# Optimization experiments

Hardware: AMD Instinct MI355X
Metric: run time of the kernel (lower is better)

The kernel has to match this reference:

```python
import jax, jax.numpy as jnp
import numpy as np

NUM_K_HEADS = 16
NUM_V_HEADS = 32
DK = 128
DV = 128
KCONV = 4
EPS = 1e-6
KEY_DIM = NUM_K_HEADS * DK      # 2048
VALUE_DIM = NUM_V_HEADS * DV    # 4096
HIDDEN = 2048
T_TOKENS = 4096


def setup_inputs() -> dict:
    key = jax.random.key(0)
    ks = jax.random.split(key, 10)
    s = 0.02
    return {
        "hidden_states": jax.random.normal(ks[0], (T_TOKENS, HIDDEN), jnp.float32),
        "W_qkv": jax.random.normal(ks[1], (2 * KEY_DIM + VALUE_DIM, HIDDEN), jnp.float32) * s,
        "W_z": jax.random.normal(ks[2], (VALUE_DIM, HIDDEN), jnp.float32) * s,
        "W_b": jax.random.normal(ks[3], (NUM_V_HEADS, HIDDEN), jnp.float32) * s,
        "W_a": jax.random.normal(ks[4], (NUM_V_HEADS, HIDDEN), jnp.float32) * s,
        "conv_weight": jax.random.normal(ks[5], (2 * KEY_DIM + VALUE_DIM, KCONV), jnp.float32) * 0.2,
        "dt_bias": jnp.ones((NUM_V_HEADS,), jnp.float32),
        "A_log": jax.random.normal(ks[6], (NUM_V_HEADS,), jnp.float32) * 0.5,
        "norm_weight": jnp.ones((DV,), jnp.float32),
        "W_out": jax.random.normal(ks[7], (HIDDEN, VALUE_DIM), jnp.float32) * s,
    }


def _l2norm(x):
    return x * jax.lax.rsqrt(jnp.sum(x * x, axis=-1, keepdims=True) + 1e-6)


def _gdn_forward(hidden_states, W_qkv, W_z, W_b, W_a, conv_weight,
                 dt_bias, A_log, norm_weight, W_out):
    T = hidden_states.shape[0]
    # input projections
    mixed_qkv = hidden_states @ W_qkv.T                         # [T, 2K+V]
    z = (hidden_states @ W_z.T).reshape(T, NUM_V_HEADS, DV)     # gate
    b = hidden_states @ W_b.T                                   # [T, Hv]
    a = hidden_states @ W_a.T                                   # [T, Hv]

    # depthwise causal conv1d (kernel 4) + silu, no bias
    xp = jnp.pad(mixed_qkv, ((KCONV - 1, 0), (0, 0)))
    conv = sum(xp[i:i + T] * conv_weight[:, i] for i in range(KCONV))
    x = jax.nn.silu(conv)

    q = x[:, :KEY_DIM].reshape(T, NUM_K_HEADS, DK)
    k = x[:, KEY_DIM:2 * KEY_DIM].reshape(T, NUM_K_HEADS, DK)
    v = x[:, 2 * KEY_DIM:].reshape(T, NUM_V_HEADS, DV)

    rep = NUM_V_HEADS // NUM_K_HEADS  # grouped value attention: repeat q/k heads
    q = jnp.repeat(_l2norm(q), rep, axis=1)  # [T, Hv, DK]
    k = jnp.repeat(_l2norm(k), rep, axis=1)

    beta = jax.nn.sigmoid(b)                                   # [T, Hv]
    g = -jnp.exp(A_log) * jax.nn.softplus(a + dt_bias)         # [T, Hv] log-decay
    scale = DK ** -0.5

    def step(S, inp):
        qt, kt, vt, bt, gt = inp
        S = S * jnp.exp(gt)[:, None, None]                     # gated decay
        kv = jnp.einsum('hk,hkv->hv', kt, S)                   # memory readout
        delta = (vt - kv) * bt[:, None]                        # delta rule update
        S = S + jnp.einsum('hk,hv->hkv', kt, delta)
        ot = jnp.einsum('hk,hkv->hv', qt, S) * scale
        return S, ot

    S0 = jnp.zeros((NUM_V_HEADS, DK, DV), mixed_qkv.dtype)
    _, o = jax.lax.scan(step, S0, (q, k, v, beta, g))          # o: [T, Hv, DV]

    # gated RMSNorm (norm before gate)
    var = jnp.mean(o * o, axis=-1, keepdims=True)
    on = o * jax.lax.rsqrt(var + EPS) * norm_weight
    y = on * jax.nn.silu(z)

    return y.reshape(T, VALUE_DIM) @ W_out.T                   # [T, HIDDEN]


def reference(hidden_states, W_qkv, W_z, W_b, W_a, conv_weight,
              dt_bias, A_log, norm_weight, W_out):
    return _gdn_forward(hidden_states, W_qkv, W_z, W_b, W_a, conv_weight,
                        dt_bias, A_log, norm_weight, W_out)
```

## Files before the change

### kernel.cpp

```cpp
#include <hip/hip_runtime.h>
#include <cstdint>
#include <cstddef>

typedef __bf16 bf16_t;
typedef __bf16 bf16x8 __attribute__((ext_vector_type(8)));
typedef __bf16 bf16x4 __attribute__((ext_vector_type(4)));
typedef float floatx4 __attribute__((ext_vector_type(4)));

__device__ __forceinline__ void async16(const bf16_t* g, bf16_t* l) {
  __builtin_amdgcn_global_load_lds(
      (const __attribute__((address_space(1))) unsigned int*)g,
      (__attribute__((address_space(3))) unsigned int*)l, 16, 0, 0);
}

__device__ __forceinline__ void barrier_lds() {
  asm volatile("s_waitcnt lgkmcnt(0)\n\ts_barrier" ::: "memory");
}

__device__ __forceinline__ float siluf(float x) { return x / (1.f + __expf(-x)); }

#define MFMA16(a, b, c) __builtin_amdgcn_mfma_f32_16x16x32_bf16(a, b, c, 0, 0, 0)

__global__ __launch_bounds__(256) void k_cvt(const float* __restrict__ in,
                                             bf16_t* __restrict__ out, int n4) {
  int i = blockIdx.x * 256 + threadIdx.x;
  if (i >= n4) return;
  const float4 f = ((const float4*)in)[i];
  bf16x4 r;
  r[0] = (bf16_t)f.x; r[1] = (bf16_t)f.y; r[2] = (bf16_t)f.z; r[3] = (bf16_t)f.w;
  ((bf16x4*)out)[i] = r;
}

__global__ __launch_bounds__(256) void k_build_wba(const float* __restrict__ wb,
                                                   const float* __restrict__ wa,
                                                   bf16_t* __restrict__ out) {
  int i = blockIdx.x * 256 + threadIdx.x;
  int e = i * 4;
  int row = e >> 11;
  int col = e & 2047;
  float4 f = make_float4(0.f, 0.f, 0.f, 0.f);
  if (row < 32)      f = *(const float4*)&wb[row * 2048 + col];
  else if (row < 64) f = *(const float4*)&wa[(row - 32) * 2048 + col];
  bf16x4 r;
  r[0] = (bf16_t)f.x; r[1] = (bf16_t)f.y; r[2] = (bf16_t)f.z; r[3] = (bf16_t)f.w;
  *(bf16x4*)&out[e] = r;
}

template<bool OUT_BF16>
__global__ __launch_bounds__(256) void gemm_bt(const bf16_t* __restrict__ A,
                                               const bf16_t* __restrict__ B,
                                               void* __restrict__ Cout,
                                               int M, int N, int K) {
  __shared__ __align__(16) bf16_t As[4096];
  __shared__ __align__(16) bf16_t Bs[4096];
  const int tid  = threadIdx.x;
  const int lane = tid & 63;
  const int wave = tid >> 6;
  const int quad = lane >> 4;
  const int l16  = lane & 15;
  const int wr   = (wave >> 1) * 64;
  const int wc   = (wave & 1) * 64;
  const int m0   = blockIdx.y * 128;
  const int n0   = blockIdx.x * 128;
  const int ra   = tid >> 2;
  const int ca   = (tid & 3) * 8;

  const bf16_t* gA = A + (size_t)(m0 + ra) * K + ca;
  const bf16_t* gB = B + (size_t)(n0 + ra) * K + ca;
  bf16_t* lA = &As[tid * 8];
  bf16_t* lB = &Bs[tid * 8];

  floatx4 acc[4][4] = {};

  for (int k0 = 0; k0 < K; k0 += 32) {
    __syncthreads();
    async16(gA + k0, lA);
    async16(gA + k0 + (size_t)64 * K, lA + 2048);
    async16(gB + k0, lB);
    async16(gB + k0 + (size_t)64 * K, lB + 2048);
    __syncthreads();
    bf16x8 af[4], bfr[4];
#pragma unroll
    for (int i = 0; i < 4; ++i) {
      af[i]  = *(const bf16x8*)&As[(wr + i * 16 + l16) * 32 + quad * 8];
      bfr[i] = *(const bf16x8*)&Bs[(wc + i * 16 + l16) * 32 + quad * 8];
    }
#pragma unroll
    for (int mi = 0; mi < 4; ++mi)
#pragma unroll
      for (int ni = 0; ni < 4; ++ni)
        acc[mi][ni] = MFMA16(af[mi], bfr[ni], acc[mi][ni]);
  }

#pragma unroll
  for (int mi = 0; mi < 4; ++mi) {
#pragma unroll
    for (int ni = 0; ni < 4; ++ni) {
      const int row = m0 + wr + mi * 16 + quad * 4;
      const int col = n0 + wc + ni * 16 + l16;
#pragma unroll
      for (int r = 0; r < 4; ++r) {
        if (OUT_BF16)
          ((bf16_t*)Cout)[(size_t)(row + r) * N + col] = (bf16_t)acc[mi][ni][r];
        else
          ((float*)Cout)[(size_t)(row + r) * N + col] = acc[mi][ni][r];
      }
    }
  }
}

template<bool OUT_BF16>
__global__ __launch_bounds__(512, 1) void gemm256(const bf16_t* __restrict__ A,
                                                  const bf16_t* __restrict__ B,
                                                  void* __restrict__ Cout,
                                                  int M, int N, int K) {
  extern __shared__ __align__(16) bf16_t sm[];
  const int tid  = threadIdx.x;
  const int lane = tid & 63;
  const int wave = tid >> 6;
  const int quad = lane >> 4;
  const int l16  = lane & 15;
  const int wm   = wave >> 2;
  const int wn   = wave & 3;

  const int gx  = (int)gridDim.x;
  const int nwg = gx * (int)gridDim.y;
  const int id  = (int)blockIdx.y * gx + (int)blockIdx.x;
  const int cpx = nwg >> 3;
  const int sw  = (id & 7) * cpx + (id >> 3);
  const int m0  = (sw / gx) * 256;
  const int n0  = (sw % gx) * 256;

  const int lr    = lane >> 2;
  const int lslot = (lane & 3) ^ ((lane >> 3) & 3);
  const bf16_t* gA = A + (size_t)(m0 + wave * 32 + lr) * K + lslot * 8;
  const bf16_t* gB = B + (size_t)(n0 + wave * 32 + lr) * K + lslot * 8;
  const int ldsA0 = wave * 1024 + lane * 8;
  const int ldsB0 = 8192 + wave * 1024 + lane * 8;

#define STG_A(u, kt) {                                          \
    bf16_t* la = sm + (u) * 16384 + ldsA0;                      \
    const bf16_t* ga = gA + (size_t)(kt) * 32;                  \
    async16(ga, la);                                            \
    async16(ga + (size_t)16 * K, la + 512); }
#define STG_B(u, kt) {                                          \
    bf16_t* lb = sm + (u) * 16384 + ldsB0;                      \
    const bf16_t* gb = gB + (size_t)(kt) * 32;                  \
    async16(gb, lb);                                            \
    async16(gb + (size_t)16 * K, lb + 512); }

  int offA[8], offB[4];
#pragma unroll
  for (int i = 0; i < 8; ++i) {
    int ra = wm * 128 + i * 16 + l16;
    offA[i] = (ra * 32 + quad * 8) ^ (((ra >> 1) & 3) << 3);
  }
#pragma unroll
  for (int i = 0; i < 4; ++i) {
    int rb = wn * 64 + i * 16 + l16;
    offB[i] = 8192 + ((rb * 32 + quad * 8) ^ (((rb >> 1) & 3) << 3));
  }

  floatx4 acc[8][4] = {};
  const int KT = K >> 5;

  STG_A(0, 0); STG_B(0, 0);
  STG_A(1, 1); STG_B(1, 1);
  STG_A(2, 2); STG_B(2, 2);
  asm volatile("s_waitcnt vmcnt(8)" ::: "memory");
  asm volatile("s_barrier" ::: "memory");

  for (int U = 0; U < KT; ++U) {
    const int bu = U & 3;
    const bf16_t* sb = sm + bu * 16384;
    const int un = U + 3;
    const int tu = un & 3;
    bf16x8 af[4], bfr[4];

#pragma unroll
    for (int i = 0; i < 4; ++i) {
      af[i]  = *(const bf16x8*)&sb[offA[i]];
      bfr[i] = *(const bf16x8*)&sb[offB[i]];
    }
    if (un < KT) STG_A(tu, un);
    asm volatile("s_barrier" ::: "memory");
    __builtin_amdgcn_s_setprio(1);
#pragma unroll
    for (int mi = 0; mi < 4; ++mi)
#pragma unroll
      for (int ni = 0; ni < 4; ++ni)
        acc[mi][ni] = MFMA16(af[mi], bfr[ni], acc[mi][ni]);
    __builtin_amdgcn_s_setprio(0);
    asm volatile("s_barrier" ::: "memory");

#pragma unroll
    for (int i = 0; i < 4; ++i) af[i] = *(const bf16x8*)&sb[offA[4 + i]];
    if (un < KT) STG_B(tu, un);
    if (un < KT)         asm volatile("s_waitcnt vmcnt(8)" ::: "memory");
    else if (U + 2 < KT) asm volatile("s_waitcnt vmcnt(4)" ::: "memory");
    else                 asm volatile("s_waitcnt vmcnt(0)" ::: "memory");
    asm volatile("s_barrier" ::: "memory");
    __builtin_amdgcn_s_setprio(1);
#pragma unroll
    for (int mi = 0; mi < 4; ++mi)
#pragma unroll
      for (int ni = 0; ni < 4; ++ni)
        acc[4 + mi][ni] = MFMA16(af[mi], bfr[ni], acc[4 + mi][ni]);
    __builtin_amdgcn_s_setprio(0);
    asm volatile("s_barrier" ::: "memory");
  }
#undef STG_A
#undef STG_B

#pragma unroll
  for (int mi = 0; mi < 8; ++mi) {
#pragma unroll
    for (int ni = 0; ni < 4; ++ni) {
      const int row = m0 + wm * 128 + mi * 16 + quad * 4;
      const int col = n0 + wn * 64 + ni * 16 + l16;
#pragma unroll
      for (int r = 0; r < 4; ++r) {
        if (OUT_BF16)
          ((bf16_t*)Cout)[(size_t)(row + r) * N + col] = (bf16_t)acc[mi][ni][r];
        else
          ((float*)Cout)[(size_t)(row + r) * N + col] = acc[mi][ni][r];
      }
    }
  }
}

__global__ __launch_bounds__(256) void k_betag(const float* __restrict__ cba,
                                               const float* __restrict__ A_log,
                                               const float* __restrict__ dtb,
                                               float* __restrict__ beta_t,
                                               float* __restrict__ g_t) {
  int i = blockIdx.x * 256 + threadIdx.x;
  int t = i >> 5, h = i & 31;
  float b = cba[t * 128 + h];
  float a = cba[t * 128 + 32 + h];
  beta_t[h * 4096 + t] = 1.f / (1.f + __expf(-b));
  float x = a + dtb[h];
  float sp = (x > 20.f) ? x : log1pf(__expf(x));
  g_t[h * 4096 + t] = -__expf(A_log[h]) * sp;
}

__global__ __launch_bounds__(64) void k_conv(const bf16_t* __restrict__ mixed,
                                             const float* __restrict__ cw,
                                             bf16_t* __restrict__ qo,
                                             bf16_t* __restrict__ ko,
                                             bf16_t* __restrict__ vo) {
  const int grp = blockIdx.x;
  const int t0 = blockIdx.y * 8;
  const int l = threadIdx.x;
  const int c0 = grp * 128 + l;
  const int c1 = c0 + 64;
  const float4 w0 = *(const float4*)&cw[c0 * 4];
  const float4 w1 = *(const float4*)&cw[c1 * 4];
  float h0[3], h1[3];
#pragma unroll
  for (int j = 0; j < 3; ++j) {
    int tt = t0 - 3 + j;
    h0[j] = (tt >= 0) ? (float)mixed[(size_t)tt * 8192 + c0] : 0.f;
    h1[j] = (tt >= 0) ? (float)mixed[(size_t)tt * 8192 + c1] : 0.f;
  }
#pragma unroll
  for (int i = 0; i < 8; ++i) {
    const int t = t0 + i;
    float x0 = (float)mixed[(size_t)t * 8192 + c0];
    float x1 = (float)mixed[(size_t)t * 8192 + c1];
    float a0 = w0.x * h0[0] + w0.y * h0[1] + w0.z * h0[2] + w0.w * x0;
    float a1 = w1.x * h1[0] + w1.y * h1[1] + w1.z * h1[2] + w1.w * x1;
    h0[0] = h0[1]; h0[1] = h0[2]; h0[2] = x0;
    h1[0] = h1[1]; h1[1] = h1[2]; h1[2] = x1;
    float v0 = siluf(a0), v1 = siluf(a1);
    if (grp < 32) {
      float s = v0 * v0 + v1 * v1;
#pragma unroll
      for (int m = 1; m < 64; m <<= 1) s += __shfl_xor(s, m);
      float r = rsqrtf(s + 1e-6f);
      if (grp < 16) {
        bf16_t* q = qo + ((size_t)t * 16 + grp) * 128;
        q[l]      = (bf16_t)(v0 * r * 0.08838834764831845f);
        q[l + 64] = (bf16_t)(v1 * r * 0.08838834764831845f);
      } else {
        bf16_t* k = ko + ((size_t)t * 16 + grp - 16) * 128;
        k[l]      = (bf16_t)(v0 * r);
        k[l + 64] = (bf16_t)(v1 * r);
      }
    } else {
      bf16_t* v = vo + ((size_t)t * 32 + grp - 32) * 128;
      v[l]      = (bf16_t)v0;
      v[l + 64] = (bf16_t)v1;
    }
  }
}

__global__ __launch_bounds__(256, 2) void k_prep(
    const bf16_t* __restrict__ qg, const bf16_t* __restrict__ kg,
    const bf16_t* __restrict__ vg,
    const float* __restrict__ bb_t, const float* __restrict__ gb_t,
    bf16_t* __restrict__ Vt, bf16_t* __restrict__ Wlo, bf16_t* __restrict__ Whi,
    bf16_t* __restrict__ Mout, bf16_t* __restrict__ kt, float* __restrict__ smalls) {
  const int c = blockIdx.x >> 5;
  const int h = blockIdx.x & 31;
  const int kh = h >> 1;
  const int t0 = c * 64;
  const int tid = threadIdx.x, lane = tid & 63, wave = tid >> 6;
  const int quad = lane >> 4, l16 = lane & 15;

  __shared__ __align__(16) bf16_t lsKQ[2][64][136];
  __shared__ float lsC[64][68];
  __shared__ float lsG[64], lsA[64], lsSc[64], lsBeta[64];

  {
    const int r = tid >> 2, s0 = (tid & 3) * 32;
    const bf16_t* kr = kg + ((size_t)(t0 + r) * 16 + kh) * 128 + s0;
    const bf16_t* qr = qg + ((size_t)(t0 + r) * 16 + kh) * 128 + s0;
#pragma unroll
    for (int j = 0; j < 4; ++j) {
      *(uint4*)&lsKQ[0][r][s0 + j * 8] = *(const uint4*)&kr[j * 8];
      *(uint4*)&lsKQ[1][r][s0 + j * 8] = *(const uint4*)&qr[j * 8];
    }
  }
  if (wave == 0) {
    float gv = gb_t[(size_t)h * 4096 + t0 + lane];
#pragma unroll
    for (int off = 1; off < 64; off <<= 1) {
      float n = __shfl_up(gv, off);
      if (lane >= off) gv += n;
    }
    float GL = __shfl(gv, 63);
    lsG[lane] = gv;
    lsA[lane] = __expf(gv);
    lsSc[lane] = __expf(GL - gv);
    lsBeta[lane] = bb_t[(size_t)h * 4096 + t0 + lane];
  }
  __syncthreads();

  const int mr = (wave >> 1) * 32, nr = (wave & 1) * 32;
  floatx4 ak[2][2] = {}, aq[2][2] = {};
  if (wave != 1) {
#pragma unroll
    for (int ks = 0; ks < 4; ++ks) {
      bf16x8 yf[2], xk[2], xq[2];
#pragma unroll
      for (int i = 0; i < 2; ++i) {
        yf[i] = *(const bf16x8*)&lsKQ[0][nr + i * 16 + l16][ks * 32 + quad * 8];
        xk[i] = *(const bf16x8*)&lsKQ[0][mr + i * 16 + l16][ks * 32 + quad * 8];
        xq[i] = *(const bf16x8*)&lsKQ[1][mr + i * 16 + l16][ks * 32 + quad * 8];
      }
#pragma unroll
      for (int i = 0; i < 2; ++i)
#pragma unroll
        for (int j = 0; j < 2; ++j) {
          ak[i][j] = MFMA16(xk[i], yf[j], ak[i][j]);
          aq[i][j] = MFMA16(xq[i], yf[j], aq[i][j]);
        }
    }
  }
  bf16_t* Mb = Mout + (size_t)(h * 64 + c) * 4096;
#pragma unroll
  for (int i = 0; i < 2; ++i)
#pragma unroll
    for (int j = 0; j < 2; ++j)
#pragma unroll
      for (int r = 0; r < 4; ++r) {
        int t = mr + i * 16 + quad * 4 + r;
        int s = nr + j * 16 + l16;
        float e = __expf(lsG[t] - lsG[s]);
        float cv = (s < t) ? lsBeta[t] * e * ak[i][j][r] : 0.f;
        float mv = (s <= t) ? e * aq[i][j][r] : 0.f;
        if (wave != 1) lsC[t][s] = cv;
        Mb[t * 64 + s] = (bf16_t)mv;
      }
  __syncthreads();

  const int col = tid & 127;
  const bool isW = tid >= 128;
  float vals[64];
#pragma unroll
  for (int t = 0; t < 64; ++t) {
    float b;
    if (!isW) b = (float)vg[((size_t)(t0 + t) * 32 + h) * 128 + col];
    else      b = lsA[t] * (float)lsKQ[0][t][col];
    vals[t] = lsBeta[t] * b;
  }
#pragma unroll
  for (int t = 1; t < 64; ++t) {
    float acc = vals[t];
#pragma unroll
    for (int s4 = 0; s4 <= (t - 1) >> 2; ++s4) {
      float4 cv = *(const float4*)&lsC[t][s4 * 4];
      acc -= cv.x * vals[s4 * 4 + 0];
      acc -= cv.y * vals[s4 * 4 + 1];
      acc -= cv.z * vals[s4 * 4 + 2];
      acc -= cv.w * vals[s4 * 4 + 3];
    }
    vals[t] = acc;
  }

  if (!isW) {
    bf16_t* vd = Vt + (size_t)(h * 64 + c) * 8192 + (size_t)col * 64;
#pragma unroll
    for (int j = 0; j < 16; ++j) {
      bf16x4 p;
      p[0] = (bf16_t)vals[j * 4 + 0];
      p[1] = (bf16_t)vals[j * 4 + 1];
      p[2] = (bf16_t)vals[j * 4 + 2];
      p[3] = (bf16_t)vals[j * 4 + 3];
      *(bf16x4*)&vd[j * 4] = p;
    }
  } else {
#pragma unroll
    for (int t = 0; t < 64; ++t) vals[t] = -vals[t];
  }

  if ((h & 1) == 0) {
    const int dk = tid >> 1, sh = (tid & 1) * 32;
    bf16_t* kd = kt + (size_t)(c * 16 + kh) * 8192 + (size_t)dk * 64 + sh;
#pragma unroll
    for (int j4 = 0; j4 < 4; ++j4) {
      bf16x8 v;
#pragma unroll
      for (int e = 0; e < 8; ++e) v[e] = lsKQ[0][sh + j4 * 8 + e][dk];
      *(bf16x8*)&kd[j4 * 8] = v;
    }
  }
  if (tid < 64) {
    float* sm = smalls + (size_t)(h * 64 + c) * 128;
    sm[tid] = lsA[tid];
    sm[64 + tid] = lsSc[tid];
  }
  __syncthreads();

  bf16_t* lsT = &lsKQ[0][0][0];
  if (isW) {
#pragma unroll
    for (int t = 0; t < 64; ++t) lsT[t * 272 + tid] = (bf16_t)vals[t];
  }
  __syncthreads();

  {
    const int r = tid >> 2, part = tid & 3;
    const bf16_t* src = &lsT[r * 272 + 128 + part * 32];
    bf16_t* Wb = (h < 16 ? Wlo : Whi) + (size_t)((h & 15) * 64 + c) * 8192 + r * 128 + part * 32;
#pragma unroll
    for (int j = 0; j < 4; ++j)
      *(uint4*)&Wb[j * 8] = *(const uint4*)&src[j * 8];
  }
}

__device__ __forceinline__ void chain_prefetch(
    int c2, int wave, int l16, int quad, int trow, int dv0, int kh,
    const bf16_t* __restrict__ Wbase, const bf16_t* __restrict__ Vbase,
    const bf16_t* __restrict__ Mbase, const bf16_t* __restrict__ qg,
    const bf16_t* __restrict__ ktg, const float* __restrict__ Sbase,
    bf16x8 nW[4], bf16x8 nQ[4], bf16x8 nK[4], bf16x8 nM[2],
    bf16x4 nV[4], float4& nA, float4& nSc, float& nAL) {
  const bf16_t* Wn = Wbase + (size_t)c2 * 8192;
  const bf16_t* Vn = Vbase + (size_t)c2 * 8192;
  const bf16_t* Qn = qg + ((size_t)(c2 * 64 + wave * 16 + l16) * 16 + kh) * 128;
  const bf16_t* Kn = ktg + (size_t)(c2 * 16 + kh) * 8192;
  const bf16_t* Mn = Mbase + (size_t)c2 * 4096 + (wave * 16 + l16) * 64;
  const float* sm = Sbase + (size_t)c2 * 128;
#pragma unroll
  for (int ks = 0; ks < 4; ++ks) {
    nW[ks] = *(const bf16x8*)&Wn[(size_t)(wave * 16 + l16) * 128 + ks * 32 + quad * 8];
    nQ[ks] = *(const bf16x8*)&Qn[ks * 32 + quad * 8];
    nK[ks] = *(const bf16x8*)&Kn[(size_t)((wave + 4 * (ks >> 1)) * 16 + l16) * 64 + (ks & 1) * 32 + quad * 8];
  }
#pragma unroll
  for (int ks = 0; ks < 2; ++ks) nM[ks] = *(const bf16x8*)&Mn[ks * 32 + quad * 8];
#pragma unroll
  for (int tn = 0; tn < 4; ++tn)
    nV[tn] = *(const bf16x4*)&Vn[(size_t)(dv0 + tn * 16 + l16) * 64 + trow];
  nA = *(const float4*)&sm[trow];
  nSc = *(const float4*)&sm[64 + trow];
  nAL = sm[63];
}

__global__ __launch_bounds__(256, 1) void k_chain(
    const bf16_t* __restrict__ qg, const bf16_t* __restrict__ VtT,
    const bf16_t* __restrict__ Wlo, const bf16_t* __restrict__ Whi,
    const bf16_t* __restrict__ Mg, const bf16_t* __restrict__ ktg,
    const float* __restrict__ smalls, bf16_t* __restrict__ o) {
  const int h = blockIdx.x & 31;
  const int dv0 = (blockIdx.x >> 5) * 64;
  const int kh = h >> 1;
  const int tid = threadIdx.x, lane = tid & 63, wave = tid >> 6;
  const int quad = lane >> 4, l16 = lane & 15;
  const int trow = wave * 16 + quad * 4;

  __shared__ __align__(16) bf16_t lsXT[64][72];
  __shared__ __align__(16) bf16_t lsXbT[64][72];
  __shared__ __align__(16) bf16_t lsS[64][136];

  const bf16_t* Wbase = (h < 16 ? Wlo : Whi) + (size_t)(h & 15) * 64 * 8192;
  const bf16_t* Vbase = VtT + (size_t)h * 64 * 8192;
  const bf16_t* Mbase = Mg + (size_t)h * 64 * 4096;
  const float*  Sbase = smalls + (size_t)h * 64 * 128;

  floatx4 sacc[2][4] = {};
  for (int i = tid; i < 64 * 136; i += 256) (&lsS[0][0])[i] = (bf16_t)0.f;

  bf16x8 nW[4], nQ[4], nK[4], nM[2];
  bf16x4 nV[4];
  float4 nA, nSc;
  float nAL;
  chain_prefetch(0, wave, l16, quad, trow, dv0, kh, Wbase, Vbase, Mbase, qg, ktg,
                 Sbase, nW, nQ, nK, nM, nV, nA, nSc, nAL);
  __syncthreads();

  for (int cc = 0; cc < 64; ++cc) {
    const int t0 = cc * 64;
    bf16x8 cW[4], cQ[4], cK[4], cM[2];
    float cV[16];
    float4 cA = nA, cSc = nSc;
    float cAL = nAL;
#pragma unroll
    for (int ks = 0; ks < 4; ++ks) { cW[ks] = nW[ks]; cQ[ks] = nQ[ks]; cK[ks] = nK[ks]; }
    cM[0] = nM[0]; cM[1] = nM[1];
#pragma unroll
    for (int tn = 0; tn < 4; ++tn)
#pragma unroll
      for (int r = 0; r < 4; ++r) cV[tn * 4 + r] = (float)nV[tn][r];

    if (cc + 1 < 64)
      chain_prefetch(cc + 1, wave, l16, quad, trow, dv0, kh, Wbase, Vbase, Mbase,
                     qg, ktg, Sbase, nW, nQ, nK, nM, nV, nA, nSc, nAL);

    bf16x8 bS[4][4];
#pragma unroll
    for (int ks = 0; ks < 4; ++ks)
#pragma unroll
      for (int tn = 0; tn < 4; ++tn)
        bS[ks][tn] = *(const bf16x8*)&lsS[tn * 16 + l16][ks * 32 + quad * 8];
    floatx4 xacc[4];
#pragma unroll
    for (int tn = 0; tn < 4; ++tn)
#pragma unroll
      for (int r = 0; r < 4; ++r) xacc[tn][r] = cV[tn * 4 + r];
#pragma unroll
    for (int ks = 0; ks < 4; ++ks)
#pragma unroll
      for (int tn = 0; tn < 4; ++tn)
        xacc[tn] = MFMA16(cW[ks], bS[ks][tn], xacc[tn]);
#pragma unroll
    for (int tn = 0; tn < 4; ++tn) {
      bf16x4 px, pb;
#pragma unroll
      for (int r = 0; r < 4; ++r) {
        px[r] = (bf16_t)xacc[tn][r];
        pb[r] = (bf16_t)(xacc[tn][r] * ((const float*)&cSc)[r]);
      }
      *(bf16x4*)&lsXT[tn * 16 + l16][trow] = px;
      *(bf16x4*)&lsXbT[tn * 16 + l16][trow] = pb;
    }
    barrier_lds();

    floatx4 qacc[4] = {};
#pragma unroll
    for (int ks = 0; ks < 4; ++ks)
#pragma unroll
      for (int tn = 0; tn < 4; ++tn)
        qacc[tn] = MFMA16(cQ[ks], bS[ks][tn], qacc[tn]);
#pragma unroll
    for (int tn = 0; tn < 4; ++tn)
#pragma unroll
      for (int r = 0; r < 4; ++r) qacc[tn][r] *= ((const float*)&cA)[r];
#pragma unroll
    for (int ks = 0; ks < 2; ++ks)
#pragma unroll
      for (int tn = 0; tn < 4; ++tn) {
        bf16x8 bX = *(const bf16x8*)&lsXT[tn * 16 + l16][ks * 32 + quad * 8];
        qacc[tn] = MFMA16(cM[ks], bX, qacc[tn]);
      }
#pragma unroll
    for (int tn = 0; tn < 4; ++tn)
#pragma unroll
      for (int r = 0; r < 4; ++r)
        o[((size_t)(t0 + trow + r) * 32 + h) * 128 + dv0 + tn * 16 + l16] =
            (bf16_t)qacc[tn][r];
#pragma unroll
    for (int mh = 0; mh < 2; ++mh)
#pragma unroll
      for (int tn = 0; tn < 4; ++tn)
#pragma unroll
        for (int r = 0; r < 4; ++r) sacc[mh][tn][r] *= cAL;
#pragma unroll
    for (int ks = 0; ks < 2; ++ks) {
      bf16x8 bXb[4];
#pragma unroll
      for (int tn = 0; tn < 4; ++tn)
        bXb[tn] = *(const bf16x8*)&lsXbT[tn * 16 + l16][ks * 32 + quad * 8];
#pragma unroll
      for (int mh = 0; mh < 2; ++mh)
#pragma unroll
        for (int tn = 0; tn < 4; ++tn)
          sacc[mh][tn] = MFMA16(cK[mh * 2 + ks], bXb[tn], sacc[mh][tn]);
    }
#pragma unroll
    for (int mh = 0; mh < 2; ++mh)
#pragma unroll
      for (int tn = 0; tn < 4; ++tn) {
        bf16x4 ps;
#pragma unroll
        for (int r = 0; r < 4; ++r) ps[r] = (bf16_t)sacc[mh][tn][r];
        *(bf16x4*)&lsS[tn * 16 + l16][(wave + 4 * mh) * 16 + quad * 4] = ps;
      }
    barrier_lds();
  }
}

__global__ __launch_bounds__(256) void k_gate(const bf16_t* __restrict__ o,
                                              const bf16_t* __restrict__ z,
                                              const float* __restrict__ nw,
                                              bf16_t* __restrict__ y) {
  const int row = blockIdx.x * 4 + (threadIdx.x >> 6);
  const int l = threadIdx.x & 63;
  const bf16_t* orow = o + (size_t)row * 128;
  float o0 = (float)orow[l], o1 = (float)orow[l + 64];
  float s = o0 * o0 + o1 * o1;
#pragma unroll
  for (int m = 1; m < 64; m <<= 1) s += __shfl_xor(s, m);
  float r = rsqrtf(s * (1.f / 128.f) + 1e-6f);
  const bf16_t* zrow = z + (size_t)row * 128;
  float z0 = (float)zrow[l], z1 = (float)zrow[l + 64];
  bf16_t* yrow = y + (size_t)row * 128;
  yrow[l]      = (bf16_t)(o0 * r * nw[l] * siluf(z0));
  yrow[l + 64] = (bf16_t)(o1 * r * nw[l + 64] * siluf(z1));
}

extern "C" void kernel_launch(void* const* d_in, const int* in_sizes, int n_in,
                              void* d_out, int out_size, void* d_ws, size_t ws_size,
                              hipStream_t stream) {
  const float* hidden = (const float*)d_in[0];
  const float* W_qkv  = (const float*)d_in[1];
  const float* W_z    = (const float*)d_in[2];
  const float* W_b    = (const float*)d_in[3];
  const float* W_a    = (const float*)d_in[4];
  const float* conv_w = (const float*)d_in[5];
  const float* dt_b   = (const float*)d_in[6];
  const float* A_log  = (const float*)d_in[7];
  const float* norm_w = (const float*)d_in[8];
  const float* W_out  = (const float*)d_in[9];
  float* out = (float*)d_out;

  static int gemm_attr_done = 0;
  if (!gemm_attr_done) {
    hipFuncSetAttribute(reinterpret_cast<const void*>(&gemm256<true>),
                        hipFuncAttributeMaxDynamicSharedMemorySize, 131072);
    hipFuncSetAttribute(reinterpret_cast<const void*>(&gemm256<false>),
                        hipFuncAttributeMaxDynamicSharedMemorySize, 131072);
    gemm_attr_done = 1;
  }

  char* w = (char*)d_ws;
  const size_t MB = 1024 * 1024;
  bf16_t* hs    = (bf16_t*)(w + 0 * MB);
  bf16_t* Wlo   = hs;
  bf16_t* wqkv  = (bf16_t*)(w + 16 * MB);
  bf16_t* Vtb   = wqkv;
  bf16_t* ybuf  = wqkv;
  bf16_t* wz    = (bf16_t*)(w + 48 * MB);
  bf16_t* Whi   = wz;
  bf16_t* wout  = (bf16_t*)(w + 64 * MB);
  bf16_t* wba   = (bf16_t*)(w + 80 * MB);
  bf16_t* mixed = (bf16_t*)(w + 81 * MB);
  bf16_t* obuf  = mixed;
  bf16_t* Mbuf  = (bf16_t*)(w + 113 * MB);
  bf16_t* ktb   = (bf16_t*)(w + 129 * MB);
  bf16_t* zbuf  = (bf16_t*)(w + 145 * MB);
  float*  cba   = (float*)(w + 177 * MB);
  float*  smalls= cba;
  bf16_t* qb    = (bf16_t*)(w + 179 * MB);
  bf16_t* kb    = (bf16_t*)(w + 195 * MB);
  bf16_t* vb    = (bf16_t*)(w + 211 * MB);
  float*  betab = (float*)(w + 243 * MB);
  float*  gbuf  = (float*)(w + 243 * MB + 512 * 1024);

  k_cvt<<<8192, 256, 0, stream>>>(hidden, hs, 2097152);
  k_cvt<<<16384, 256, 0, stream>>>(W_qkv, wqkv, 4194304);
  k_cvt<<<8192, 256, 0, stream>>>(W_z, wz, 2097152);
  k_cvt<<<8192, 256, 0, stream>>>(W_out, wout, 2097152);
  k_build_wba<<<256, 256, 0, stream>>>(W_b, W_a, wba);

  gemm256<true><<<dim3(32, 16), 512, 131072, stream>>>(hs, wqkv, mixed, 4096, 8192, 2048);
  gemm256<true><<<dim3(16, 16), 512, 131072, stream>>>(hs, wz, zbuf, 4096, 4096, 2048);
  gemm_bt<false><<<dim3(1, 32), 256, 0, stream>>>(hs, wba, cba, 4096, 128, 2048);
  k_betag<<<512, 256, 0, stream>>>(cba, A_log, dt_b, betab, gbuf);

  k_conv<<<dim3(64, 512), 64, 0, stream>>>(mixed, conv_w, qb, kb, vb);

  k_prep<<<2048, 256, 0, stream>>>(qb, kb, vb, betab, gbuf,
                                   Vtb, Wlo, Whi, Mbuf, ktb, smalls);
  k_chain<<<64, 256, 0, stream>>>(qb, Vtb, Wlo, Whi, Mbuf, ktb, smalls, obuf);

  k_gate<<<32768, 256, 0, stream>>>(obuf, zbuf, norm_w, ybuf);
  gemm_bt<false><<<dim3(16, 32), 256, 0, stream>>>(ybuf, wout, out, 4096, 2048, 4096);
}
```

Before: 904.3 us.

## Split chunk-recurrence work across eight waves per block in k_chain

The sequential chunked delta-rule kernel now launches 512 threads per block instead of 256. The dv columns are split between wave pairs, and each wave owns a 16-row slice of the state update. This halves per-wave MFMA and register work on the serial critical path, and the prefetch helper is replaced by incrementing pointers. Only 64 blocks run, so the aim is more latency hiding per CU. The cost is more barrier participants, and the same Q, W and M fragments are loaded redundantly by the paired waves.

```diff
diff --git a/kernel.cpp b/kernel.cpp
--- a/kernel.cpp
+++ b/kernel.cpp
@@ -450,36 +450,7 @@
   }
 }
 
-__device__ __forceinline__ void chain_prefetch(
-    int c2, int wave, int l16, int quad, int trow, int dv0, int kh,
-    const bf16_t* __restrict__ Wbase, const bf16_t* __restrict__ Vbase,
-    const bf16_t* __restrict__ Mbase, const bf16_t* __restrict__ qg,
-    const bf16_t* __restrict__ ktg, const float* __restrict__ Sbase,
-    bf16x8 nW[4], bf16x8 nQ[4], bf16x8 nK[4], bf16x8 nM[2],
-    bf16x4 nV[4], float4& nA, float4& nSc, float& nAL) {
-  const bf16_t* Wn = Wbase + (size_t)c2 * 8192;
-  const bf16_t* Vn = Vbase + (size_t)c2 * 8192;
-  const bf16_t* Qn = qg + ((size_t)(c2 * 64 + wave * 16 + l16) * 16 + kh) * 128;
-  const bf16_t* Kn = ktg + (size_t)(c2 * 16 + kh) * 8192;
-  const bf16_t* Mn = Mbase + (size_t)c2 * 4096 + (wave * 16 + l16) * 64;
-  const float* sm = Sbase + (size_t)c2 * 128;
-#pragma unroll
-  for (int ks = 0; ks < 4; ++ks) {
-    nW[ks] = *(const bf16x8*)&Wn[(size_t)(wave * 16 + l16) * 128 + ks * 32 + quad * 8];
-    nQ[ks] = *(const bf16x8*)&Qn[ks * 32 + quad * 8];
-    nK[ks] = *(const bf16x8*)&Kn[(size_t)((wave + 4 * (ks >> 1)) * 16 + l16) * 64 + (ks & 1) * 32 + quad * 8];
-  }
-#pragma unroll
-  for (int ks = 0; ks < 2; ++ks) nM[ks] = *(const bf16x8*)&Mn[ks * 32 + quad * 8];
-#pragma unroll
-  for (int tn = 0; tn < 4; ++tn)
-    nV[tn] = *(const bf16x4*)&Vn[(size_t)(dv0 + tn * 16 + l16) * 64 + trow];
-  nA = *(const float4*)&sm[trow];
-  nSc = *(const float4*)&sm[64 + trow];
-  nAL = sm[63];
-}
-
-__global__ __launch_bounds__(256, 1) void k_chain(
+__global__ __launch_bounds__(512, 2) void k_chain(
     const bf16_t* __restrict__ qg, const bf16_t* __restrict__ VtT,
     const bf16_t* __restrict__ Wlo, const bf16_t* __restrict__ Whi,
     const bf16_t* __restrict__ Mg, const bf16_t* __restrict__ ktg,
@@ -489,7 +460,10 @@
   const int kh = h >> 1;
   const int tid = threadIdx.x, lane = tid & 63, wave = tid >> 6;
   const int quad = lane >> 4, l16 = lane & 15;
-  const int trow = wave * 16 + quad * 4;
+  const int wt = wave >> 1;
+  const int wv = wave & 1;
+  const int trow = wt * 16 + quad * 4;
+  const int dkr = wave * 16;
 
   __shared__ __align__(16) bf16_t lsXT[64][72];
   __shared__ __align__(16) bf16_t lsXbT[64][72];
@@ -500,114 +474,148 @@
   const bf16_t* Mbase = Mg + (size_t)h * 64 * 4096;
   const float*  Sbase = smalls + (size_t)h * 64 * 128;
 
-  floatx4 sacc[2][4] = {};
-  for (int i = tid; i < 64 * 136; i += 256) (&lsS[0][0])[i] = (bf16_t)0.f;
-
-  bf16x8 nW[4], nQ[4], nK[4], nM[2];
-  bf16x4 nV[4];
+  const bf16_t* pW = Wbase + (size_t)(wt * 16 + l16) * 128 + quad * 8;
+  const bf16_t* pQ = qg + ((size_t)(wt * 16 + l16) * 16 + kh) * 128 + quad * 8;
+  const bf16_t* pK = ktg + (size_t)kh * 8192 + (size_t)(dkr + l16) * 64 + quad * 8;
+  const bf16_t* pM = Mbase + (size_t)(wt * 16 + l16) * 64 + quad * 8;
+  const bf16_t* pV = Vbase + (size_t)(dv0 + wv * 32 + l16) * 64 + trow;
+  const float*  pS = Sbase;
+
+  floatx4 sacc[4] = {};
+  for (int i = tid; i < 64 * 136; i += 512) (&lsS[0][0])[i] = (bf16_t)0.f;
+
+  bf16x8 nW[4], nQ[4], nK[2], nM[2];
+  bf16x4 nV[2];
   float4 nA, nSc;
   float nAL;
-  chain_prefetch(0, wave, l16, quad, trow, dv0, kh, Wbase, Vbase, Mbase, qg, ktg,
-                 Sbase, nW, nQ, nK, nM, nV, nA, nSc, nAL);
+  {
+#pragma unroll
+    for (int ks = 0; ks < 4; ++ks) {
+      nW[ks] = *(const bf16x8*)&pW[ks * 32];
+      nQ[ks] = *(const bf16x8*)&pQ[ks * 32];
+    }
+#pragma unroll
+    for (int j = 0; j < 2; ++j) {
+      nK[j] = *(const bf16x8*)&pK[j * 32];
+      nM[j] = *(const bf16x8*)&pM[j * 32];
+    }
+#pragma unroll
+    for (int tn = 0; tn < 2; ++tn) nV[tn] = *(const bf16x4*)&pV[tn * 1024];
+    nA  = *(const float4*)&pS[trow];
+    nSc = *(const float4*)&pS[64 + trow];
+    nAL = pS[63];
+    pW += 8192; pQ += 131072; pK += 131072; pM += 4096; pV += 8192; pS += 128;
+  }
   __syncthreads();
 
   for (int cc = 0; cc < 64; ++cc) {
     const int t0 = cc * 64;
-    bf16x8 cW[4], cQ[4], cK[4], cM[2];
-    float cV[16];
+    bf16x8 cW[4], cQ[4], cK[2], cM[2];
+    float cV[8];
     float4 cA = nA, cSc = nSc;
     float cAL = nAL;
 #pragma unroll
-    for (int ks = 0; ks < 4; ++ks) { cW[ks] = nW[ks]; cQ[ks] = nQ[ks]; cK[ks] = nK[ks]; }
+    for (int ks = 0; ks < 4; ++ks) { cW[ks] = nW[ks]; cQ[ks] = nQ[ks]; }
+    cK[0] = nK[0]; cK[1] = nK[1];
     cM[0] = nM[0]; cM[1] = nM[1];
 #pragma unroll
-    for (int tn = 0; tn < 4; ++tn)
+    for (int tn = 0; tn < 2; ++tn)
 #pragma unroll
       for (int r = 0; r < 4; ++r) cV[tn * 4 + r] = (float)nV[tn][r];
 
-    if (cc + 1 < 64)
-      chain_prefetch(cc + 1, wave, l16, quad, trow, dv0, kh, Wbase, Vbase, Mbase,
-                     qg, ktg, Sbase, nW, nQ, nK, nM, nV, nA, nSc, nAL);
-
-    bf16x8 bS[4][4];
+    if (cc + 1 < 64) {
+#pragma unroll
+      for (int ks = 0; ks < 4; ++ks) {
+        nW[ks] = *(const bf16x8*)&pW[ks * 32];
+        nQ[ks] = *(const bf16x8*)&pQ[ks * 32];
+      }
+#pragma unroll
+      for (int j = 0; j < 2; ++j) {
+        nK[j] = *(const bf16x8*)&pK[j * 32];
+        nM[j] = *(const bf16x8*)&pM[j * 32];
+      }
+#pragma unroll
+      for (int tn = 0; tn < 2; ++tn) nV[tn] = *(const bf16x4*)&pV[tn * 1024];
+      nA  = *(const float4*)&pS[trow];
+      nSc = *(const float4*)&pS[64 + trow];
+      nAL = pS[63];
+      pW += 8192; pQ += 131072; pK += 131072; pM += 4096; pV += 8192; pS += 128;
+    }
+
+    bf16x8 bS[4][2];
 #pragma unroll
     for (int ks = 0; ks < 4; ++ks)
 #pragma unroll
-      for (int tn = 0; tn < 4; ++tn)
-        bS[ks][tn] = *(const bf16x8*)&lsS[tn * 16 + l16][ks * 32 + quad * 8];
-    floatx4 xacc[4];
-#pragma unroll
-    for (int tn = 0; tn < 4; ++tn)
+      for (int tn = 0; tn < 2; ++tn)
+        bS[ks][tn] = *(const bf16x8*)&lsS[wv * 32 + tn * 16 + l16][ks * 32 + quad * 8];
+    floatx4 xacc[2];
+#pragma unroll
+    for (int tn = 0; tn < 2; ++tn)
 #pragma unroll
       for (int r = 0; r < 4; ++r) xacc[tn][r] = cV[tn * 4 + r];
 #pragma unroll
     for (int ks = 0; ks < 4; ++ks)
 #pragma unroll
-      for (int tn = 0; tn < 4; ++tn)
+      for (int tn = 0; tn < 2; ++tn)
         xacc[tn] = MFMA16(cW[ks], bS[ks][tn], xacc[tn]);
 #pragma unroll
-    for (int tn = 0; tn < 4; ++tn) {
+    for (int tn = 0; tn < 2; ++tn) {
       bf16x4 px, pb;
 #pragma unroll
       for (int r = 0; r < 4; ++r) {
         px[r] = (bf16_t)xacc[tn][r];
         pb[r] = (bf16_t)(xacc[tn][r] * ((const float*)&cSc)[r]);
       }
-      *(bf16x4*)&lsXT[tn * 16 + l16][trow] = px;
-      *(bf16x4*)&lsXbT[tn * 16 + l16][trow] = pb;
+      *(bf16x4*)&lsXT[wv * 32 + tn * 16 + l16][trow] = px;
+      *(bf16x4*)&lsXbT[wv * 32 + tn * 16 + l16][trow] = pb;
     }
     barrier_lds();
 
-    floatx4 qacc[4] = {};
+    floatx4 qacc[2] = {};
 #pragma unroll
     for (int ks = 0; ks < 4; ++ks)
 #pragma unroll
+      for (int tn = 0; tn < 2; ++tn)
+        qacc[tn] = MFMA16(cQ[ks], bS[ks][tn], qacc[tn]);
+#pragma unroll
+    for (int tn = 0; tn < 2; ++tn)
+#pragma unroll
+      for (int r = 0; r < 4; ++r) qacc[tn][r] *= ((const float*)&cA)[r];
+#pragma unroll
+    for (int j = 0; j < 2; ++j)
+#pragma unroll
+      for (int tn = 0; tn < 2; ++tn) {
+        bf16x8 bX = *(const bf16x8*)&lsXT[wv * 32 + tn * 16 + l16][j * 32 + quad * 8];
+        qacc[tn] = MFMA16(cM[j], bX, qacc[tn]);
+      }
+#pragma unroll
+    for (int tn = 0; tn < 2; ++tn)
+#pragma unroll
+      for (int r = 0; r < 4; ++r)
+        o[((size_t)(t0 + trow + r) * 32 + h) * 128 + dv0 + wv * 32 + tn * 16 + l16] =
+            (bf16_t)qacc[tn][r];
+
+#pragma unroll
+    for (int tn = 0; tn < 4; ++tn)
+#pragma unroll
+      for (int r = 0; r < 4; ++r) sacc[tn][r] *= cAL;
+#pragma unroll
+    for (int j = 0; j < 2; ++j) {
+      bf16x8 bXb[4];
+#pragma unroll
       for (int tn = 0; tn < 4; ++tn)
-        qacc[tn] = MFMA16(cQ[ks], bS[ks][tn], qacc[tn]);
-#pragma unroll
-    for (int tn = 0; tn < 4; ++tn)
-#pragma unroll
-      for (int r = 0; r < 4; ++r) qacc[tn][r] *= ((const float*)&cA)[r];
-#pragma unroll
-    for (int ks = 0; ks < 2; ++ks)
-#pragma unroll
-      for (int tn = 0; tn < 4; ++tn) {
-        bf16x8 bX = *(const bf16x8*)&lsXT[tn * 16 + l16][ks * 32 + quad * 8];
-        qacc[tn] = MFMA16(cM[ks], bX, qacc[tn]);
-      }
-#pragma unroll
-    for (int tn = 0; tn < 4; ++tn)
-#pragma unroll
-      for (int r = 0; r < 4; ++r)
-        o[((size_t)(t0 + trow + r) * 32 + h) * 128 + dv0 + tn * 16 + l16] =
-            (bf16_t)qacc[tn][r];
-#pragma unroll
-    for (int mh = 0; mh < 2; ++mh)
+        bXb[tn] = *(const bf16x8*)&lsXbT[tn * 16 + l16][j * 32 + quad * 8];
 #pragma unroll
       for (int tn = 0; tn < 4; ++tn)
-#pragma unroll
-        for (int r = 0; r < 4; ++r) sacc[mh][tn][r] *= cAL;
-#pragma unroll
-    for (int ks = 0; ks < 2; ++ks) {
-      bf16x8 bXb[4];
-#pragma unroll
-      for (int tn = 0; tn < 4; ++tn)
-        bXb[tn] = *(const bf16x8*)&lsXbT[tn * 16 + l16][ks * 32 + quad * 8];
-#pragma unroll
-      for (int mh = 0; mh < 2; ++mh)
-#pragma unroll
-        for (int tn = 0; tn < 4; ++tn)
-          sacc[mh][tn] = MFMA16(cK[mh * 2 + ks], bXb[tn], sacc[mh][tn]);
-    }
-#pragma unroll
-    for (int mh = 0; mh < 2; ++mh)
-#pragma unroll
-      for (int tn = 0; tn < 4; ++tn) {
-        bf16x4 ps;
-#pragma unroll
-        for (int r = 0; r < 4; ++r) ps[r] = (bf16_t)sacc[mh][tn][r];
-        *(bf16x4*)&lsS[tn * 16 + l16][(wave + 4 * mh) * 16 + quad * 4] = ps;
-      }
+        sacc[tn] = MFMA16(cK[j], bXb[tn], sacc[tn]);
+    }
+#pragma unroll
+    for (int tn = 0; tn < 4; ++tn) {
+      bf16x4 ps;
+#pragma unroll
+      for (int r = 0; r < 4; ++r) ps[r] = (bf16_t)sacc[tn][r];
+      *(bf16x4*)&lsS[tn * 16 + l16][dkr + quad * 4] = ps;
+    }
     barrier_lds();
   }
 }
@@ -694,7 +702,7 @@
 
   k_prep<<<2048, 256, 0, stream>>>(qb, kb, vb, betab, gbuf,
                                    Vtb, Wlo, Whi, Mbuf, ktb, smalls);
-  k_chain<<<64, 256, 0, stream>>>(qb, Vtb, Wlo, Whi, Mbuf, ktb, smalls, obuf);
+  k_chain<<<64, 512, 0, stream>>>(qb, Vtb, Wlo, Whi, Mbuf, ktb, smalls, obuf);
 
   k_gate<<<32768, 256, 0, stream>>>(obuf, zbuf, norm_w, ybuf);
   gemm_bt<false><<<dim3(16, 32), 256, 0, stream>>>(ybuf, wout, out, 4096, 2048, 4096);
```

New measurement: 968.3 us. 7.1% more time.
